# Optimization experiments

Hardware: AMD Instinct MI355X
Metric: run time of the kernel (lower is better)

## Reference

```python
import jax, jax.numpy as jnp
import numpy as np

USER = 100000
ITEM = 200000
N = USER + ITEM
LATDIM = 64
N_LAYERS = 3
N_EDGES = 4800000


def spmm(rows, cols, vals, x):
    # out[r] = sum_e vals[e] * x[cols[e]] for edges with rows[e] == r
    msgs = vals[:, None] * x[cols]  # [E, D]
    return jax.ops.segment_sum(msgs, rows, num_segments=N)


def setup_inputs() -> dict:
    key = jax.random.key(0)
    k1, k2, k3, k4, k5 = jax.random.split(key, 5)
    adj_rows = jax.random.randint(k1, (N_EDGES,), 0, N, dtype=jnp.int32)
    adj_cols = jax.random.randint(k2, (N_EDGES,), 0, N, dtype=jnp.int32)
    adj_vals = jax.random.uniform(k3, (N_EDGES,), dtype=jnp.float32)
    uEmbeds = jax.random.normal(k4, (USER, LATDIM), dtype=jnp.float32)
    iEmbeds = jax.random.normal(k5, (ITEM, LATDIM), dtype=jnp.float32)
    return {"adj_rows": adj_rows, "adj_cols": adj_cols, "adj_vals": adj_vals,
            "uEmbeds": uEmbeds, "iEmbeds": iEmbeds}


def reference(adj_rows, adj_cols, adj_vals, uEmbeds, iEmbeds):
    embeds = jnp.concatenate([uEmbeds, iEmbeds], axis=0)  # [N, D]
    acc = embeds  # sum pooling accumulator (layer 0)
    for _ in range(N_LAYERS):
        embeds = spmm(adj_rows, adj_cols, adj_vals, embeds)
        acc = acc + embeds
    # pool='sum' over stacked layer outputs == running sum above
    return acc[:USER], acc[USER:]
```

## Files before the change

### kernel.cpp

```cpp
#include <hip/hip_runtime.h>

#define D 64
#define AB_SHIFT 9
#define AROWS 512
#define NAB_MAX 640
#define CHP 3
#define P_EPB 4096
#define P_T 256
#define P_PER (P_EPB / P_T)
#define SORT_T 512
#define SORT_CAP 9472
#define BSTRIDE 8704
#define VSCALE 8192.0f
#define VINV   (1.0f / 8192.0f)

__device__ __forceinline__ unsigned short f2bf(float f) {
    unsigned u = __float_as_uint(f);
    return (unsigned short)((u + 0x7FFFu + ((u >> 16) & 1u)) >> 16);
}
__device__ __forceinline__ float bflo(unsigned u) {
    return __uint_as_float(u << 16);
}
__device__ __forceinline__ float bfhi(unsigned u) {
    return __uint_as_float(u & 0xFFFF0000u);
}

__global__ __launch_bounds__(256) void conv_init(
    const float* __restrict__ u, const float* __restrict__ it,
    unsigned short* __restrict__ q, long long userD, long long totalD,
    int* __restrict__ gcur, int nab)
{
    int g = blockIdx.x * 256 + threadIdx.x;
    if (g < nab) gcur[g] = g * BSTRIDE;
    long long stride = (long long)gridDim.x * 256 * 4;
    for (long long i = ((long long)blockIdx.x * 256 + threadIdx.x) * 4;
         i < totalD; i += stride) {
        float4 x = (i < userD) ? *(const float4*)(u + i)
                               : *(const float4*)(it + (i - userD));
        ushort4 o;
        o.x = f2bf(x.x); o.y = f2bf(x.y); o.z = f2bf(x.z); o.w = f2bf(x.w);
        *(ushort4*)(q + i) = o;
    }
}

__global__ __launch_bounds__(P_T) void partition_edges(
    const int* __restrict__ rows, const int* __restrict__ cols,
    const float* __restrict__ vals, int* __restrict__ gcur,
    int2* __restrict__ staged, int nedges, int nab)
{
    __shared__ int h[NAB_MAX];
    __shared__ int lofs[NAB_MAX];
    __shared__ int partial[P_T];
    __shared__ int mcount;
    __shared__ int2 sbuf[P_EPB];
    __shared__ unsigned short bid[P_EPB];
    int t = threadIdx.x;
    int base = blockIdx.x * P_EPB;
    for (int i = t; i < nab; i += P_T) h[i] = 0;
    __syncthreads();
    int pk[P_PER];
    #pragma unroll
    for (int i = 0; i < P_PER; i++) {
        int e = base + i * P_T + t;
        if (e < nedges) {
            int r = rows[e];
            int b = r >> AB_SHIFT;
            int rank = atomicAdd(&h[b], 1);
            pk[i] = (rank << 19) | ((r & (AROWS - 1)) << 10) | b;
        } else pk[i] = -1;
    }
    __syncthreads();
    int s = 0;
    int b0 = t * CHP;
    #pragma unroll
    for (int j = 0; j < CHP; j++) { int b = b0 + j; if (b < nab) s += h[b]; }
    partial[t] = s;
    __syncthreads();
    for (int ofs = 1; ofs < P_T; ofs <<= 1) {
        int x = (t >= ofs) ? partial[t - ofs] : 0;
        __syncthreads();
        partial[t] += x;
        __syncthreads();
    }
    if (t == P_T - 1) mcount = partial[t];
    int run = partial[t] - s;
    #pragma unroll
    for (int j = 0; j < CHP; j++) {
        int b = b0 + j;
        if (b < nab) { lofs[b] = run; run += h[b]; }
    }
    __syncthreads();
    for (int i = t; i < nab; i += P_T) {
        int c = h[i];
        if (c) { int gb = atomicAdd(&gcur[i], c); h[i] = gb - lofs[i]; }
    }
    __syncthreads();
    #pragma unroll
    for (int i = 0; i < P_PER; i++) {
        if (pk[i] < 0) continue;
        int e = base + i * P_T + t;
        int b = pk[i] & 1023;
        int rl = (pk[i] >> 10) & (AROWS - 1);
        int rank = (unsigned)pk[i] >> 19;
        int q = lofs[b] + rank;
        sbuf[q] = make_int2((rl << 19) | cols[e], __float_as_int(vals[e]));
        bid[q] = (unsigned short)b;
    }
    __syncthreads();
    int m = mcount;
    for (int q = t; q < m; q += P_T) {
        int b = bid[q];
        staged[h[b] + q] = sbuf[q];
    }
}

__global__ __launch_bounds__(SORT_T) void bucket_sort(
    const int* __restrict__ gcur, const int2* __restrict__ staged,
    unsigned* __restrict__ pairs, int* __restrict__ endp, int n)
{
    __shared__ int cnt[AROWS];
    __shared__ int pfx[AROWS];
    __shared__ unsigned buf[SORT_CAP];
    int t = threadIdx.x;
    int b = blockIdx.x;
    int seg0 = b * BSTRIDE;
    int seg1 = gcur[b];
    int len = seg1 - seg0;
    if (len > BSTRIDE) len = BSTRIDE;
    cnt[t] = 0;
    __syncthreads();
    for (int i = t; i < len; i += SORT_T) {
        int rl = (unsigned)staged[seg0 + i].x >> 19;
        atomicAdd(&cnt[rl], 1);
    }
    __syncthreads();
    pfx[t] = cnt[t];
    __syncthreads();
    for (int ofs = 1; ofs < AROWS; ofs <<= 1) {
        int x = (t >= ofs) ? pfx[t - ofs] : 0;
        __syncthreads();
        pfx[t] += x;
        __syncthreads();
    }
    int rowbase = b << AB_SHIFT;
    if (rowbase + t < n) endp[rowbase + t] = seg0 + pfx[t];
    cnt[t] = pfx[t] - cnt[t];
    __syncthreads();
    for (int i = t; i < len; i += SORT_T) {
        int2 p = staged[seg0 + i];
        int rl = (unsigned)p.x >> 19;
        int pos = atomicAdd(&cnt[rl], 1);
        float val = __int_as_float(p.y);
        unsigned q = (unsigned)fminf(val * VSCALE + 0.5f, 8191.0f);
        unsigned rec = (q << 19) | ((unsigned)p.x & 0x7FFFF);
        if (pos < SORT_CAP) buf[pos] = rec;
        else pairs[seg0 + pos] = rec;
    }
    __syncthreads();
    int m = len < SORT_CAP ? len : SORT_CAP;
    for (int i = t; i < m; i += SORT_T) pairs[seg0 + i] = buf[i];
}

__device__ __forceinline__ void gather_row(
    const int* __restrict__ endp, const unsigned* __restrict__ pairs,
    const uint4* __restrict__ tb, int row, int l,
    float& a0, float& a1, float& a2, float& a3,
    float& a4, float& a5, float& a6, float& a7)
{
    int start = (row & (AROWS - 1)) ? endp[row - 1] : (row >> AB_SHIFT) * BSTRIDE;
    int end = endp[row];
    int e = start;
    for (; e + 4 <= end; e += 4) {
        unsigned p0 = pairs[e], p1 = pairs[e + 1], p2 = pairs[e + 2], p3 = pairs[e + 3];
        uint4 q0 = tb[(size_t)(p0 & 0x7FFFF) * 8 + l];
        uint4 q1 = tb[(size_t)(p1 & 0x7FFFF) * 8 + l];
        uint4 q2 = tb[(size_t)(p2 & 0x7FFFF) * 8 + l];
        uint4 q3 = tb[(size_t)(p3 & 0x7FFFF) * 8 + l];
        float v0 = (float)(p0 >> 19) * VINV;
        float v1 = (float)(p1 >> 19) * VINV;
        float v2 = (float)(p2 >> 19) * VINV;
        float v3 = (float)(p3 >> 19) * VINV;
        a0 = fmaf(v0, bflo(q0.x), a0); a1 = fmaf(v0, bfhi(q0.x), a1);
        a2 = fmaf(v0, bflo(q0.y), a2); a3 = fmaf(v0, bfhi(q0.y), a3);
        a4 = fmaf(v0, bflo(q0.z), a4); a5 = fmaf(v0, bfhi(q0.z), a5);
        a6 = fmaf(v0, bflo(q0.w), a6); a7 = fmaf(v0, bfhi(q0.w), a7);
        a0 = fmaf(v1, bflo(q1.x), a0); a1 = fmaf(v1, bfhi(q1.x), a1);
        a2 = fmaf(v1, bflo(q1.y), a2); a3 = fmaf(v1, bfhi(q1.y), a3);
        a4 = fmaf(v1, bflo(q1.z), a4); a5 = fmaf(v1, bfhi(q1.z), a5);
        a6 = fmaf(v1, bflo(q1.w), a6); a7 = fmaf(v1, bfhi(q1.w), a7);
        a0 = fmaf(v2, bflo(q2.x), a0); a1 = fmaf(v2, bfhi(q2.x), a1);
        a2 = fmaf(v2, bflo(q2.y), a2); a3 = fmaf(v2, bfhi(q2.y), a3);
        a4 = fmaf(v2, bflo(q2.z), a4); a5 = fmaf(v2, bfhi(q2.z), a5);
        a6 = fmaf(v2, bflo(q2.w), a6); a7 = fmaf(v2, bfhi(q2.w), a7);
        a0 = fmaf(v3, bflo(q3.x), a0); a1 = fmaf(v3, bfhi(q3.x), a1);
        a2 = fmaf(v3, bflo(q3.y), a2); a3 = fmaf(v3, bfhi(q3.y), a3);
        a4 = fmaf(v3, bflo(q3.z), a4); a5 = fmaf(v3, bfhi(q3.z), a5);
        a6 = fmaf(v3, bflo(q3.w), a6); a7 = fmaf(v3, bfhi(q3.w), a7);
    }
    for (; e < end; ++e) {
        unsigned p = pairs[e];
        uint4 q0 = tb[(size_t)(p & 0x7FFFF) * 8 + l];
        float v = (float)(p >> 19) * VINV;
        a0 = fmaf(v, bflo(q0.x), a0); a1 = fmaf(v, bfhi(q0.x), a1);
        a2 = fmaf(v, bflo(q0.y), a2); a3 = fmaf(v, bfhi(q0.y), a3);
        a4 = fmaf(v, bflo(q0.z), a4); a5 = fmaf(v, bfhi(q0.z), a5);
        a6 = fmaf(v, bflo(q0.w), a6); a7 = fmaf(v, bfhi(q0.w), a7);
    }
}

__global__ __launch_bounds__(256) void spmm_mid(
    const int* __restrict__ endp, const unsigned* __restrict__ pairs,
    const unsigned short* __restrict__ tab,
    unsigned short* __restrict__ outq, int n)
{
    int row = blockIdx.x * 32 + (threadIdx.x >> 3);
    if (row >= n) return;
    int l = threadIdx.x & 7;
    float a0=0.f,a1=0.f,a2=0.f,a3=0.f,a4=0.f,a5=0.f,a6=0.f,a7=0.f;
    gather_row(endp, pairs, (const uint4*)tab, row, l, a0,a1,a2,a3,a4,a5,a6,a7);
    uint4 o;
    o.x = ((unsigned)f2bf(a1) << 16) | f2bf(a0);
    o.y = ((unsigned)f2bf(a3) << 16) | f2bf(a2);
    o.z = ((unsigned)f2bf(a5) << 16) | f2bf(a4);
    o.w = ((unsigned)f2bf(a7) << 16) | f2bf(a6);
    *(uint4*)(outq + (size_t)row * D + l * 8) = o;
}

__global__ __launch_bounds__(256) void spmm_final(
    const int* __restrict__ endp, const unsigned* __restrict__ pairs,
    const unsigned short* __restrict__ e2q, const unsigned short* __restrict__ e1q,
    const unsigned short* __restrict__ e0q,
    const float* __restrict__ u, const float* __restrict__ it, int user,
    float* __restrict__ acc, int n)
{
    int row = blockIdx.x * 32 + (threadIdx.x >> 3);
    if (row >= n) return;
    int l = threadIdx.x & 7;
    float a0=0.f,a1=0.f,a2=0.f,a3=0.f,a4=0.f,a5=0.f,a6=0.f,a7=0.f;
    gather_row(endp, pairs, (const uint4*)e2q, row, l, a0,a1,a2,a3,a4,a5,a6,a7);
    size_t off = (size_t)row * D + l * 8;
    float4 b0, b1;
    if (e0q) {
        uint4 q0 = *(const uint4*)(e0q + off);
        b0 = make_float4(bflo(q0.x), bfhi(q0.x), bflo(q0.y), bfhi(q0.y));
        b1 = make_float4(bflo(q0.z), bfhi(q0.z), bflo(q0.w), bfhi(q0.w));
    } else {
        const float* e0 = ((row < user) ? u + (size_t)row * D
                                        : it + (size_t)(row - user) * D) + l * 8;
        b0 = *(const float4*)e0;
        b1 = *(const float4*)(e0 + 4);
    }
    uint4 q1 = *(const uint4*)(e1q + off);
    uint4 q2 = *(const uint4*)(e2q + off);
    float4 r0, r1;
    r0.x = a0 + b0.x + bflo(q1.x) + bflo(q2.x);
    r0.y = a1 + b0.y + bfhi(q1.x) + bfhi(q2.x);
    r0.z = a2 + b0.z + bflo(q1.y) + bflo(q2.y);
    r0.w = a3 + b0.w + bfhi(q1.y) + bfhi(q2.y);
    r1.x = a4 + b1.x + bflo(q1.z) + bflo(q2.z);
    r1.y = a5 + b1.y + bfhi(q1.z) + bfhi(q2.z);
    r1.z = a6 + b1.z + bflo(q1.w) + bflo(q2.w);
    r1.w = a7 + b1.w + bfhi(q1.w) + bfhi(q2.w);
    *(float4*)(acc + off) = r0;
    *(float4*)(acc + off + 4) = r1;
}

static inline size_t alignup(size_t x) { return (x + 255) & ~(size_t)255; }

extern "C" void kernel_launch(void* const* d_in, const int* in_sizes, int n_in,
                              void* d_out, int out_size, void* d_ws, size_t ws_size,
                              hipStream_t stream) {
    const int*   rows = (const int*)  d_in[0];
    const int*   cols = (const int*)  d_in[1];
    const float* vals = (const float*)d_in[2];
    const float* u    = (const float*)d_in[3];
    const float* it   = (const float*)d_in[4];

    const int nedges = in_sizes[0];
    const int user   = in_sizes[3] / D;
    const int item   = in_sizes[4] / D;
    const int n      = user + item;
    const int nab    = (n + AROWS - 1) >> AB_SHIFT;
    const size_t nslots = (size_t)nab * BSTRIDE + 8192;

    float* acc = (float*)d_out;

    char* w0 = (char*)d_ws;
    char* w = w0;
    int*  gcur = (int*)w;  w += alignup((size_t)nab * sizeof(int));
    int*  endp = (int*)w;  w += alignup((size_t)n * sizeof(int));
    unsigned* pairs = (unsigned*)w; w += alignup(nslots * sizeof(unsigned));
    size_t stagedSz = alignup(nslots * sizeof(int2));
    size_t e1sz     = alignup((size_t)n * D * 2);
    size_t regXsz   = stagedSz > e1sz ? stagedSz : e1sz;
    char* regX = w;         w += alignup(regXsz);
    char* regY = w;         w += alignup((size_t)n * D * 2);
    char* regZ = w;         w += alignup((size_t)n * D * 2);
    const bool sep_e0 = ((size_t)(w - w0) <= ws_size);

    int2* staged = (int2*)regX;
    unsigned short* e1q = (unsigned short*)regX;
    unsigned short* e2q = (unsigned short*)regY;
    unsigned short* e0q = sep_e0 ? (unsigned short*)regZ
                                 : (unsigned short*)regY;

    const int pblocks = (nedges + P_EPB - 1) / P_EPB;
    const int sblocks = (n + 31) / 32;
    const long long userD = (long long)user * D;
    const long long totalD = (long long)n * D;

    conv_init<<<2048, 256, 0, stream>>>(u, it, e0q, userD, totalD, gcur, nab);
    partition_edges<<<pblocks, P_T, 0, stream>>>(rows, cols, vals, gcur,
                                                 staged, nedges, nab);
    bucket_sort<<<nab, SORT_T, 0, stream>>>(gcur, staged, pairs, endp, n);

    spmm_mid<<<sblocks, 256, 0, stream>>>(endp, pairs, e0q, e1q, n);
    spmm_mid<<<sblocks, 256, 0, stream>>>(endp, pairs, e1q, e2q, n);
    spmm_final<<<sblocks, 256, 0, stream>>>(
        endp, pairs, e2q, e1q, sep_e0 ? e0q : nullptr, u, it, user, acc, n);
}
```

Baseline: 416.8 us.

## Fuse bf16 conversion into partition and first SpMM layer into bucket sort

The standalone conversion kernel is removed. The fp32-to-bf16 embedding conversion now runs as a grid-stride tail of the edge-partition kernel, and the bucket cursors are zeroed with a memset, with the bucket base offset added inside the atomic. The bucket-sort kernel now also computes the first propagation layer for its 512 rows, reading the sorted edge records straight from shared memory. This drops one kernel launch and one global pass over pairs and endp. The cost is that the fused layer runs with only 64 rows in flight per 512-thread block under heavy shared-memory use, which may hide gather latency worse than the separate SpMM kernel. Output buffers are also reassigned so the first layer's result does not overwrite staged data while it is still being read.

```diff
diff --git a/kernel.cpp b/kernel.cpp
--- a/kernel.cpp
+++ b/kernel.cpp
@@ -25,28 +25,18 @@
     return __uint_as_float(u & 0xFFFF0000u);
 }
 
-__global__ __launch_bounds__(256) void conv_init(
-    const float* __restrict__ u, const float* __restrict__ it,
-    unsigned short* __restrict__ q, long long userD, long long totalD,
-    int* __restrict__ gcur, int nab)
-{
-    int g = blockIdx.x * 256 + threadIdx.x;
-    if (g < nab) gcur[g] = g * BSTRIDE;
-    long long stride = (long long)gridDim.x * 256 * 4;
-    for (long long i = ((long long)blockIdx.x * 256 + threadIdx.x) * 4;
-         i < totalD; i += stride) {
-        float4 x = (i < userD) ? *(const float4*)(u + i)
-                               : *(const float4*)(it + (i - userD));
-        ushort4 o;
-        o.x = f2bf(x.x); o.y = f2bf(x.y); o.z = f2bf(x.z); o.w = f2bf(x.w);
-        *(ushort4*)(q + i) = o;
-    }
-}
-
-__global__ __launch_bounds__(P_T) void partition_edges(
+#define FMA8(v, q) do { \
+    a0 = fmaf(v, bflo((q).x), a0); a1 = fmaf(v, bfhi((q).x), a1); \
+    a2 = fmaf(v, bflo((q).y), a2); a3 = fmaf(v, bfhi((q).y), a3); \
+    a4 = fmaf(v, bflo((q).z), a4); a5 = fmaf(v, bfhi((q).z), a5); \
+    a6 = fmaf(v, bflo((q).w), a6); a7 = fmaf(v, bfhi((q).w), a7); } while (0)
+
+__global__ __launch_bounds__(P_T) void part_conv(
     const int* __restrict__ rows, const int* __restrict__ cols,
     const float* __restrict__ vals, int* __restrict__ gcur,
-    int2* __restrict__ staged, int nedges, int nab)
+    int2* __restrict__ staged, int nedges, int nab,
+    const float* __restrict__ u, const float* __restrict__ it,
+    unsigned short* __restrict__ e0q, long long userD, long long totalD)
 {
     __shared__ int h[NAB_MAX];
     __shared__ int lofs[NAB_MAX];
@@ -92,7 +82,10 @@
     __syncthreads();
     for (int i = t; i < nab; i += P_T) {
         int c = h[i];
-        if (c) { int gb = atomicAdd(&gcur[i], c); h[i] = gb - lofs[i]; }
+        if (c) {
+            int gb = atomicAdd(&gcur[i], c) + i * BSTRIDE;
+            h[i] = gb - lofs[i];
+        }
     }
     __syncthreads();
     #pragma unroll
@@ -112,11 +105,20 @@
         int b = bid[q];
         staged[h[b] + q] = sbuf[q];
     }
-}
-
-__global__ __launch_bounds__(SORT_T) void bucket_sort(
+    long long stride = (long long)gridDim.x * P_T * 4;
+    for (long long i = ((long long)blockIdx.x * P_T + t) * 4; i < totalD; i += stride) {
+        float4 x = (i < userD) ? *(const float4*)(u + i)
+                               : *(const float4*)(it + (i - userD));
+        ushort4 o;
+        o.x = f2bf(x.x); o.y = f2bf(x.y); o.z = f2bf(x.z); o.w = f2bf(x.w);
+        *(ushort4*)(e0q + i) = o;
+    }
+}
+
+__global__ __launch_bounds__(SORT_T) void sort_g1(
     const int* __restrict__ gcur, const int2* __restrict__ staged,
-    unsigned* __restrict__ pairs, int* __restrict__ endp, int n)
+    unsigned* __restrict__ pairs, int* __restrict__ endp,
+    const unsigned short* __restrict__ e0q, unsigned short* __restrict__ e1q, int n)
 {
     __shared__ int cnt[AROWS];
     __shared__ int pfx[AROWS];
@@ -124,8 +126,7 @@
     int t = threadIdx.x;
     int b = blockIdx.x;
     int seg0 = b * BSTRIDE;
-    int seg1 = gcur[b];
-    int len = seg1 - seg0;
+    int len = gcur[b];
     if (len > BSTRIDE) len = BSTRIDE;
     cnt[t] = 0;
     __syncthreads();
@@ -157,8 +158,42 @@
         else pairs[seg0 + pos] = rec;
     }
     __syncthreads();
-    int m = len < SORT_CAP ? len : SORT_CAP;
-    for (int i = t; i < m; i += SORT_T) pairs[seg0 + i] = buf[i];
+    for (int i = t; i < len; i += SORT_T) pairs[seg0 + i] = buf[i];
+    const uint4* tb = (const uint4*)e0q;
+    int l = t & 7;
+    int wr = t >> 3;
+    for (int r = wr; r < AROWS; r += SORT_T / 8) {
+        int row = rowbase + r;
+        if (row >= n) break;
+        int ls = r ? pfx[r - 1] : 0;
+        int le = pfx[r];
+        float a0=0.f,a1=0.f,a2=0.f,a3=0.f,a4=0.f,a5=0.f,a6=0.f,a7=0.f;
+        int e = ls;
+        for (; e + 4 <= le; e += 4) {
+            unsigned p0 = buf[e], p1 = buf[e+1], p2 = buf[e+2], p3 = buf[e+3];
+            uint4 q0 = tb[(size_t)(p0 & 0x7FFFF) * 8 + l];
+            uint4 q1 = tb[(size_t)(p1 & 0x7FFFF) * 8 + l];
+            uint4 q2 = tb[(size_t)(p2 & 0x7FFFF) * 8 + l];
+            uint4 q3 = tb[(size_t)(p3 & 0x7FFFF) * 8 + l];
+            float v0 = (float)(p0 >> 19) * VINV;
+            float v1 = (float)(p1 >> 19) * VINV;
+            float v2 = (float)(p2 >> 19) * VINV;
+            float v3 = (float)(p3 >> 19) * VINV;
+            FMA8(v0, q0); FMA8(v1, q1); FMA8(v2, q2); FMA8(v3, q3);
+        }
+        for (; e < le; ++e) {
+            unsigned p = buf[e];
+            uint4 q0 = tb[(size_t)(p & 0x7FFFF) * 8 + l];
+            float v = (float)(p >> 19) * VINV;
+            FMA8(v, q0);
+        }
+        uint4 o;
+        o.x = ((unsigned)f2bf(a1) << 16) | f2bf(a0);
+        o.y = ((unsigned)f2bf(a3) << 16) | f2bf(a2);
+        o.z = ((unsigned)f2bf(a5) << 16) | f2bf(a4);
+        o.w = ((unsigned)f2bf(a7) << 16) | f2bf(a6);
+        *(uint4*)(e1q + (size_t)row * D + l * 8) = o;
+    }
 }
 
 __device__ __forceinline__ void gather_row(
@@ -180,31 +215,13 @@
         float v1 = (float)(p1 >> 19) * VINV;
         float v2 = (float)(p2 >> 19) * VINV;
         float v3 = (float)(p3 >> 19) * VINV;
-        a0 = fmaf(v0, bflo(q0.x), a0); a1 = fmaf(v0, bfhi(q0.x), a1);
-        a2 = fmaf(v0, bflo(q0.y), a2); a3 = fmaf(v0, bfhi(q0.y), a3);
-        a4 = fmaf(v0, bflo(q0.z), a4); a5 = fmaf(v0, bfhi(q0.z), a5);
-        a6 = fmaf(v0, bflo(q0.w), a6); a7 = fmaf(v0, bfhi(q0.w), a7);
-        a0 = fmaf(v1, bflo(q1.x), a0); a1 = fmaf(v1, bfhi(q1.x), a1);
-        a2 = fmaf(v1, bflo(q1.y), a2); a3 = fmaf(v1, bfhi(q1.y), a3);
-        a4 = fmaf(v1, bflo(q1.z), a4); a5 = fmaf(v1, bfhi(q1.z), a5);
-        a6 = fmaf(v1, bflo(q1.w), a6); a7 = fmaf(v1, bfhi(q1.w), a7);
-        a0 = fmaf(v2, bflo(q2.x), a0); a1 = fmaf(v2, bfhi(q2.x), a1);
-        a2 = fmaf(v2, bflo(q2.y), a2); a3 = fmaf(v2, bfhi(q2.y), a3);
-        a4 = fmaf(v2, bflo(q2.z), a4); a5 = fmaf(v2, bfhi(q2.z), a5);
-        a6 = fmaf(v2, bflo(q2.w), a6); a7 = fmaf(v2, bfhi(q2.w), a7);
-        a0 = fmaf(v3, bflo(q3.x), a0); a1 = fmaf(v3, bfhi(q3.x), a1);
-        a2 = fmaf(v3, bflo(q3.y), a2); a3 = fmaf(v3, bfhi(q3.y), a3);
-        a4 = fmaf(v3, bflo(q3.z), a4); a5 = fmaf(v3, bfhi(q3.z), a5);
-        a6 = fmaf(v3, bflo(q3.w), a6); a7 = fmaf(v3, bfhi(q3.w), a7);
+        FMA8(v0, q0); FMA8(v1, q1); FMA8(v2, q2); FMA8(v3, q3);
     }
     for (; e < end; ++e) {
         unsigned p = pairs[e];
         uint4 q0 = tb[(size_t)(p & 0x7FFFF) * 8 + l];
         float v = (float)(p >> 19) * VINV;
-        a0 = fmaf(v, bflo(q0.x), a0); a1 = fmaf(v, bfhi(q0.x), a1);
-        a2 = fmaf(v, bflo(q0.y), a2); a3 = fmaf(v, bfhi(q0.y), a3);
-        a4 = fmaf(v, bflo(q0.z), a4); a5 = fmaf(v, bfhi(q0.z), a5);
-        a6 = fmaf(v, bflo(q0.w), a6); a7 = fmaf(v, bfhi(q0.w), a7);
+        FMA8(v, q0);
     }
 }
 
@@ -304,18 +321,19 @@
     unsigned short* e0q = sep_e0 ? (unsigned short*)regZ
                                  : (unsigned short*)regY;
 
+    unsigned short* E1 = sep_e0 ? (unsigned short*)regY : e1q;
+    unsigned short* E2 = sep_e0 ? (unsigned short*)regX : e2q;
+
     const int pblocks = (nedges + P_EPB - 1) / P_EPB;
     const int sblocks = (n + 31) / 32;
     const long long userD = (long long)user * D;
     const long long totalD = (long long)n * D;
 
-    conv_init<<<2048, 256, 0, stream>>>(u, it, e0q, userD, totalD, gcur, nab);
-    partition_edges<<<pblocks, P_T, 0, stream>>>(rows, cols, vals, gcur,
-                                                 staged, nedges, nab);
-    bucket_sort<<<nab, SORT_T, 0, stream>>>(gcur, staged, pairs, endp, n);
-
-    spmm_mid<<<sblocks, 256, 0, stream>>>(endp, pairs, e0q, e1q, n);
-    spmm_mid<<<sblocks, 256, 0, stream>>>(endp, pairs, e1q, e2q, n);
+    hipMemsetAsync(gcur, 0, (size_t)nab * sizeof(int), stream);
+    part_conv<<<pblocks, P_T, 0, stream>>>(rows, cols, vals, gcur, staged,
+                                           nedges, nab, u, it, e0q, userD, totalD);
+    sort_g1<<<nab, SORT_T, 0, stream>>>(gcur, staged, pairs, endp, e0q, E1, n);
+    spmm_mid<<<sblocks, 256, 0, stream>>>(endp, pairs, E1, E2, n);
     spmm_final<<<sblocks, 256, 0, stream>>>(
-        endp, pairs, e2q, e1q, sep_e0 ? e0q : nullptr, u, it, user, acc, n);
-}
+        endp, pairs, E2, E1, sep_e0 ? e0q : nullptr, u, it, user, acc, n);
+}
```

New measurement: 426.6 us. 1.02x slower.
